# Kernel optimization log

Hardware: AMD Instinct MI355X
Metric: run time of the kernel (lower is better)

## Reference

```python
import jax, jax.numpy as jnp
import numpy as np

B, C, H, W = 32, 256, 32, 32
N_EMBED = 8192
BETA = 0.25  # used for the (unreturned) commitment loss in the original


def setup_inputs() -> dict:
    key = jax.random.key(0)
    k1, k2 = jax.random.split(key)
    z = jax.random.normal(k1, (B, C, H, W), dtype=jnp.float32)
    embedding = jax.random.normal(k2, (N_EMBED, C), dtype=jnp.float32)
    return {"z": z, "embedding": embedding}


def reference(z, embedding):
    # z: [b, c, h, w] -> [b, h, w, c] -> [N, d]
    b, c, h, w = z.shape
    z_bhwc = jnp.transpose(z, (0, 2, 3, 1))
    z_flat = z_bhwc.reshape(-1, c)  # [N, d]

    # Squared L2 distance to every codebook entry: [N, n_embed]
    d = (
        jnp.sum(z_flat * z_flat, axis=1, keepdims=True)
        + jnp.sum(embedding * embedding, axis=1)
        - 2.0 * jnp.einsum("nd,kd->nk", z_flat, embedding)
    )
    min_encoding_indices = jnp.argmin(d, axis=1)  # [N] int

    # Codebook gather + straight-through estimator
    z_q = embedding[min_encoding_indices].reshape(b, h, w, c)
    z_q = z_bhwc + jax.lax.stop_gradient(z_q - z_bhwc)
    z_q = jnp.transpose(z_q, (0, 3, 1, 2))  # back to [b, c, h, w]
    return z_q, min_encoding_indices
```

## Files before the change

kernel.cpp:

```cpp
#include <hip/hip_runtime.h>

#define BATCH   32
#define CDIM    256
#define HWSZ    1024
#define NTOK    32768
#define KEMB    8192
#define ZQ_SIZE (BATCH * CDIM * HWSZ)

typedef short bf16x8 __attribute__((ext_vector_type(8)));
typedef float floatx4 __attribute__((ext_vector_type(4)));

#define MSPLIT 4
#define STRIP  (KEMB / MSPLIT)
#define MB8    128
#define NB8    128
#define MT8    (STRIP / MB8)

#define WS8_ESQ   0ULL
#define WS8_EQM   32768ULL
#define WS8_EH    65536ULL
#define WS8_ZH    4259840ULL
#define WS8_ZL    21037056ULL
#define WS8_PART  37814272ULL
#define WS8_IDX   39911424ULL
#define WS8_TOTAL 40042496ULL

__device__ __forceinline__ unsigned short bf16rne(float f) {
    unsigned int u = __float_as_uint(f);
    return (unsigned short)((u + 0x7fffu + ((u >> 16) & 1u)) >> 16);
}
__device__ __forceinline__ unsigned int packsplit(float f) {
    unsigned int u  = __float_as_uint(f);
    unsigned int hi = (u + 0x7fffu + ((u >> 16) & 1u)) >> 16;
    float rest      = f - __uint_as_float(hi << 16);
    unsigned int u2 = __float_as_uint(rest);
    unsigned int lo = (u2 + 0x7fffu + ((u2 >> 16) & 1u)) >> 16;
    return (hi << 16) | lo;
}
__device__ __forceinline__ unsigned umin32(unsigned a, unsigned b) { return a < b ? a : b; }
__device__ __forceinline__ unsigned umax32(unsigned a, unsigned b) { return a > b ? a : b; }

#define GLOAD_LDS16(g, l) \
    __builtin_amdgcn_global_load_lds((const __attribute__((address_space(1))) void*)(g), \
                                     (__attribute__((address_space(3))) void*)(l), 16, 0, 0)

__global__ void esqcvt_kernel(const float* __restrict__ emb, float* __restrict__ eSq,
                              float* __restrict__ eqm, unsigned short* __restrict__ eh) {
    int k    = blockIdx.x * 4 + (threadIdx.x >> 6);
    int lane = threadIdx.x & 63;
    float4 v = *(const float4*)&emb[k * CDIM + lane * 4];
    float s  = v.x * v.x + v.y * v.y + v.z * v.z + v.w * v.w;
    #pragma unroll
    for (int off = 32; off; off >>= 1) s += __shfl_down(s, off);
    ushort4 h = make_ushort4(bf16rne(v.x), bf16rne(v.y), bf16rne(v.z), bf16rne(v.w));
    *(ushort4*)&eh[k * CDIM + lane * 4] = h;
    if (lane == 0) { eSq[k] = s; eqm[k] = s * 2048.0f + 8388608.0f; }
}

__global__ void splitz_kernel(const float* __restrict__ z, unsigned short* __restrict__ zh,
                              unsigned short* __restrict__ zl) {
    __shared__ unsigned int tile[64][65];
    int b  = blockIdx.x >> 6;
    int r  = blockIdx.x & 63;
    int dt = r >> 4, ht = r & 15;
    int t  = threadIdx.x;
    #pragma unroll
    for (int i = 0; i < 4; ++i) {
        int u  = t + 256 * i;
        int dr = u >> 4;
        int c4 = (u & 15) * 4;
        float4 v = *(const float4*)&z[(((size_t)(b * 256 + dt * 64 + dr)) << 10) + ht * 64 + c4];
        tile[dr][c4 + 0] = packsplit(v.x);
        tile[dr][c4 + 1] = packsplit(v.y);
        tile[dr][c4 + 2] = packsplit(v.z);
        tile[dr][c4 + 3] = packsplit(v.w);
    }
    __syncthreads();
    #pragma unroll
    for (int i = 0; i < 2; ++i) {
        int u  = t + 256 * i;
        int tr = u & 63;
        int d8 = u >> 6;
        unsigned short h8[8], l8[8];
        #pragma unroll
        for (int j = 0; j < 8; ++j) {
            unsigned int p = tile[d8 * 8 + j][tr];
            h8[j] = (unsigned short)(p >> 16);
            l8[j] = (unsigned short)(p & 0xffff);
        }
        size_t off = (size_t)(b * 1024 + ht * 64 + tr) * 256 + dt * 64 + d8 * 8;
        *(uint4*)&zh[off] = *(uint4*)h8;
        *(uint4*)&zl[off] = *(uint4*)l8;
    }
}

#define EQOFF 49152u

#define ISSUE_A(rn, bo_) do { \
    const char* ga_ = gA0 + (size_t)((rn) >> 2) * 65536 + (size_t)((rn) & 3) * 128; \
    _Pragma("unroll") \
    for (int j_ = 0; j_ < 4; ++j_) \
        GLOAD_LDS16(ga_ + j_ * 4096, lds + (bo_) + wvOff + j_ * 1024); \
} while (0)

#define MFMA_ROUND(dr_, bo_) do { \
    __builtin_amdgcn_s_setprio(1); \
    _Pragma("unroll") \
    for (int dk_ = 0; dk_ < 2; ++dk_) { \
        const unsigned xoff_ = (bo_) + (((unsigned)(dk_ * 4) + (unsigned)quad) ^ cx) * 16; \
        bf16x8 afr_[4]; \
        _Pragma("unroll") \
        for (int rf_ = 0; rf_ < 4; ++rf_) afr_[rf_] = *(const bf16x8*)(lds + aR[rf_] + xoff_); \
        _Pragma("unroll") \
        for (int rf_ = 0; rf_ < 4; ++rf_) \
            _Pragma("unroll") \
            for (int cf_ = 0; cf_ < 4; ++cf_) \
                acc[rf_][cf_] = __builtin_amdgcn_mfma_f32_16x16x32_bf16(afr_[rf_], bfr[cf_][dr_][dk_], acc[rf_][cf_], 0, 0, 0); \
    } \
    __builtin_amdgcn_s_setprio(0); \
} while (0)

#define TOP3_EPI(mt_) do { \
    _Pragma("unroll") \
    for (int rf_ = 0; rf_ < 4; ++rf_) { \
        const unsigned base_ = (unsigned)((mt_) * MB8 + wm * 64 + rf_ * 16 + quad * 4); \
        floatx4 eq = *(const floatx4*)(lds + EQOFF + (base_ << 2)); \
        _Pragma("unroll") \
        for (int cf_ = 0; cf_ < 4; ++cf_) { \
            _Pragma("unroll") \
            for (int rr_ = 0; rr_ < 4; ++rr_) { \
                float kf = fmaf(acc[rf_][cf_][rr_], -4096.f, eq[rr_]); \
                unsigned key = (__float_as_uint(kf) << 11) | (base_ + (unsigned)rr_); \
                unsigned m1 = umax32(k1[cf_], key); \
                k1[cf_] = umin32(k1[cf_], key); \
                unsigned m2 = umax32(k2[cf_], m1); \
                k2[cf_] = umin32(k2[cf_], m1); \
                k3[cf_] = umin32(k3[cf_], m2); \
            } \
        } \
    } \
} while (0)

#define VMW4()  asm volatile("s_waitcnt vmcnt(4)" ::: "memory")
#define VMW0()  asm volatile("s_waitcnt vmcnt(0)" ::: "memory")
#define BARR()  asm volatile("s_barrier" ::: "memory")

__global__ __launch_bounds__(256, 2)
void dist8_kernel(const unsigned short* __restrict__ zhp,
                  const unsigned short* __restrict__ ehp,
                  const float* __restrict__ eqm,
                  uint4* __restrict__ part) {
    __shared__ __align__(16) char lds[57344];

    const int t    = threadIdx.x;
    const int lane = t & 63;
    const int wv   = t >> 6;
    const int wm   = wv >> 1, wn = wv & 1;
    const int l15  = lane & 15, quad = lane >> 4;

    const int nb = blockIdx.x & 255;
    const int q  = blockIdx.x >> 8;
    const int n0 = nb * NB8;
    const int cstrip = q * STRIP;

    const int dmaRow  = lane >> 3;
    const int dmaChnk = (lane & 7) ^ dmaRow;
    const unsigned laneGoff = (unsigned)dmaRow * 512 + (unsigned)dmaChnk * 16;

    const char* gA0 = (const char*)ehp + (size_t)(cstrip + wv * 32) * 512 + laneGoff;
    const char* gB0 = (const char*)zhp + (size_t)(n0 + wv * 32) * 512 + laneGoff;
    const unsigned wvOff = (unsigned)wv * 4096;
    const unsigned cx = (unsigned)(l15 & 7);

    bf16x8 bfr[4][4][2];

    #pragma unroll
    for (int s = 0; s < 2; ++s)
        #pragma unroll
        for (int j = 0; j < 4; ++j)
            GLOAD_LDS16(gB0 + s * 128 + j * 4096, lds + s * 16384 + wvOff + j * 1024);
    #pragma unroll
    for (int j = 0; j < 2; ++j)
        GLOAD_LDS16((const char*)(eqm + cstrip) + wv * 2048 + j * 1024 + lane * 16,
                    lds + EQOFF + (unsigned)wv * 2048 + (unsigned)j * 1024);
    __syncthreads();
    #pragma unroll
    for (int cf = 0; cf < 4; ++cf) {
        const unsigned bRow = (unsigned)(wn * 64 + cf * 16 + l15) * 128;
        #pragma unroll
        for (int s = 0; s < 2; ++s)
            #pragma unroll
            for (int dk = 0; dk < 2; ++dk)
                bfr[cf][s][dk] = *(const bf16x8*)(lds + s * 16384 + bRow +
                                    (((unsigned)(dk * 4) + (unsigned)quad) ^ cx) * 16);
    }
    __syncthreads();
    #pragma unroll
    for (int s = 0; s < 2; ++s)
        #pragma unroll
        for (int j = 0; j < 4; ++j)
            GLOAD_LDS16(gB0 + (s + 2) * 128 + j * 4096, lds + s * 16384 + wvOff + j * 1024);
    __syncthreads();
    #pragma unroll
    for (int cf = 0; cf < 4; ++cf) {
        const unsigned bRow = (unsigned)(wn * 64 + cf * 16 + l15) * 128;
        #pragma unroll
        for (int s = 0; s < 2; ++s)
            #pragma unroll
            for (int dk = 0; dk < 2; ++dk)
                bfr[cf][s + 2][dk] = *(const bf16x8*)(lds + s * 16384 + bRow +
                                    (((unsigned)(dk * 4) + (unsigned)quad) ^ cx) * 16);
    }
    __syncthreads();

    unsigned aR[4];
    #pragma unroll
    for (int rf = 0; rf < 4; ++rf) aR[rf] = (unsigned)(wm * 64 + rf * 16 + l15) * 128;

    unsigned k1[4], k2[4], k3[4];
    #pragma unroll
    for (int cf = 0; cf < 4; ++cf) { k1[cf] = 0xFFFFFFFFu; k2[cf] = 0xFFFFFFFFu; k3[cf] = 0xFFFFFFFFu; }

    ISSUE_A(0, 0u);
    ISSUE_A(1, 16384u);

    unsigned bufR = 0u;
    for (int mt = 0; mt < MT8 - 1; ++mt) {
        floatx4 acc[4][4];
        #pragma unroll
        for (int rf = 0; rf < 4; ++rf)
            #pragma unroll
            for (int cf = 0; cf < 4; ++cf) acc[rf][cf] = (floatx4){0.f, 0.f, 0.f, 0.f};

        #pragma unroll
        for (int dr = 0; dr < 4; ++dr) {
            VMW4();
            BARR();
            const unsigned bufI = (bufR == 0u) ? 32768u : bufR - 16384u;
            ISSUE_A(mt * 4 + dr + 2, bufI);
            MFMA_ROUND(dr, bufR);
            bufR = (bufR == 32768u) ? 0u : bufR + 16384u;
        }
        TOP3_EPI(mt);
    }
    {
        floatx4 acc[4][4];
        #pragma unroll
        for (int rf = 0; rf < 4; ++rf)
            #pragma unroll
            for (int cf = 0; cf < 4; ++cf) acc[rf][cf] = (floatx4){0.f, 0.f, 0.f, 0.f};

        VMW4(); BARR();
        { const unsigned bufI = (bufR == 0u) ? 32768u : bufR - 16384u; ISSUE_A(62, bufI); }
        MFMA_ROUND(0, bufR);
        bufR = (bufR == 32768u) ? 0u : bufR + 16384u;

        VMW4(); BARR();
        { const unsigned bufI = (bufR == 0u) ? 32768u : bufR - 16384u; ISSUE_A(63, bufI); }
        MFMA_ROUND(1, bufR);
        bufR = (bufR == 32768u) ? 0u : bufR + 16384u;

        VMW4(); BARR();
        MFMA_ROUND(2, bufR);
        bufR = (bufR == 32768u) ? 0u : bufR + 16384u;

        VMW0(); BARR();
        MFMA_ROUND(3, bufR);

        TOP3_EPI(15);
    }

    #pragma unroll
    for (int cf = 0; cf < 4; ++cf) {
        #pragma unroll
        for (int s = 0; s < 2; ++s) {
            int m = s ? 32 : 16;
            unsigned o1 = (unsigned)__shfl((int)k1[cf], lane ^ m, 64);
            unsigned o2 = (unsigned)__shfl((int)k2[cf], lane ^ m, 64);
            unsigned o3 = (unsigned)__shfl((int)k3[cf], lane ^ m, 64);
            unsigned a1  = umax32(k1[cf], o1);
            k1[cf]       = umin32(k1[cf], o1);
            unsigned b1  = umin32(k2[cf], o2);
            unsigned r3a = umax32(a1, b1);
            k2[cf]       = umin32(a1, b1);
            k3[cf]       = umin32(r3a, umin32(k3[cf], o3));
        }
    }

    __syncthreads();
    uint4* red = (uint4*)lds;
    if (quad == 0) {
        #pragma unroll
        for (int cf = 0; cf < 4; ++cf)
            red[wm * 128 + wn * 64 + cf * 16 + l15] = make_uint4(k1[cf], k2[cf], k3[cf], 0u);
    }
    __syncthreads();
    if (t < 128) {
        uint4 a = red[t], b = red[128 + t];
        unsigned a1  = umax32(a.x, b.x);
        unsigned r1  = umin32(a.x, b.x);
        unsigned b1  = umin32(a.y, b.y);
        unsigned r3a = umax32(a1, b1);
        unsigned r2  = umin32(a1, b1);
        unsigned r3  = umin32(r3a, umin32(a.z, b.z));
        part[q * NTOK + n0 + t] = make_uint4(r1, r2, r3, 0u);
    }
}

__global__ void rescore12_kernel(const unsigned short* __restrict__ zh,
                                 const unsigned short* __restrict__ zl,
                                 const float* __restrict__ emb,
                                 const float* __restrict__ eSq, const uint4* __restrict__ part,
                                 int* __restrict__ idx, float* __restrict__ idxF) {
    int n    = blockIdx.x * 4 + (threadIdx.x >> 6);
    int lane = threadIdx.x & 63;
    int c[12];
    #pragma unroll
    for (int s = 0; s < 4; ++s) {
        uint4 p = part[s * NTOK + n];
        c[3 * s]     = s * STRIP + (int)(p.x & 0x7FFu);
        c[3 * s + 1] = s * STRIP + (int)(p.y & 0x7FFu);
        c[3 * s + 2] = s * STRIP + (int)(p.z & 0x7FFu);
    }
    ushort4 h = *(const ushort4*)&zh[(size_t)n * CDIM + lane * 4];
    ushort4 l = *(const ushort4*)&zl[(size_t)n * CDIM + lane * 4];
    float z0 = __uint_as_float((unsigned)h.x << 16) + __uint_as_float((unsigned)l.x << 16);
    float z1 = __uint_as_float((unsigned)h.y << 16) + __uint_as_float((unsigned)l.y << 16);
    float z2 = __uint_as_float((unsigned)h.z << 16) + __uint_as_float((unsigned)l.z << 16);
    float z3 = __uint_as_float((unsigned)h.w << 16) + __uint_as_float((unsigned)l.w << 16);
    float acc[12];
    #pragma unroll
    for (int s = 0; s < 12; ++s) {
        float4 e = *(const float4*)&emb[(size_t)c[s] * CDIM + lane * 4];
        acc[s] = fmaf(z0, e.x, fmaf(z1, e.y, fmaf(z2, e.z, z3 * e.w)));
    }
    #pragma unroll
    for (int off = 32; off; off >>= 1) {
        #pragma unroll
        for (int s = 0; s < 12; ++s) acc[s] += __shfl_down(acc[s], off);
    }
    if (lane == 0) {
        float bd = 3.4e38f; int bi = 0x7fffffff;
        #pragma unroll
        for (int s = 0; s < 12; ++s) {
            float dv = eSq[c[s]] - 2.f * acc[s];
            if (dv < bd || (dv == bd && c[s] < bi)) { bd = dv; bi = c[s]; }
        }
        idx[n]  = bi;
        idxF[n] = (float)bi;
    }
}

__global__ void gather2_kernel(const float* __restrict__ emb, const int* __restrict__ idx,
                               float* __restrict__ out) {
    __shared__ float tile[32 * 260];
    __shared__ int rows[32];
    const int t  = threadIdx.x;
    const int n0 = blockIdx.x * 32;
    if (t < 32) rows[t] = idx[n0 + t];
    __syncthreads();
    {
        int r  = t >> 3;
        int c0 = (t & 7) * 32;
        const float* src = emb + (size_t)rows[r] * CDIM + c0;
        #pragma unroll
        for (int j = 0; j < 8; ++j) {
            float4 v = *(const float4*)(src + j * 4);
            *(float4*)&tile[r * 260 + c0 + j * 4] = v;
        }
    }
    __syncthreads();
    const int b   = n0 >> 10;
    const int hw0 = n0 & 1023;
    const int cg  = t >> 3;
    const int h4  = (t & 7) * 4;
    #pragma unroll
    for (int j = 0; j < 8; ++j) {
        int c = cg + j * 32;
        float4 v;
        v.x = tile[(h4 + 0) * 260 + c];
        v.y = tile[(h4 + 1) * 260 + c];
        v.z = tile[(h4 + 2) * 260 + c];
        v.w = tile[(h4 + 3) * 260 + c];
        *(float4*)&out[((size_t)b << 18) | ((size_t)c << 10) | (size_t)(hw0 + h4)] = v;
    }
}

#define F_BM  128
#define F_BK  128
#define F_BD  32
#define F_BSS (F_BK + 4)
#define F_KSPLIT 4
#define F_KPER  (KEMB / F_KSPLIT)
#define FWS_ESQ 0
#define FWS_PV  32768
#define FWS_PI  557056
#define FWS_IDX 1081344

__global__ void esq_kernel(const float* __restrict__ emb, float* __restrict__ eSq) {
    int k    = blockIdx.x * 4 + (threadIdx.x >> 6);
    int lane = threadIdx.x & 63;
    float4 v = *(const float4*)&emb[k * CDIM + lane * 4];
    float s  = v.x * v.x + v.y * v.y + v.z * v.z + v.w * v.w;
    #pragma unroll
    for (int off = 32; off; off >>= 1) s += __shfl_down(s, off);
    if (lane == 0) eSq[k] = s;
}

__global__ void dist_kernel(const float* __restrict__ z, const float* __restrict__ emb,
                            const float* __restrict__ eSq,
                            float* __restrict__ pv, int* __restrict__ pi) {
    __shared__ __align__(16) char smem[(F_BD * F_BM + F_BD * F_BSS) * 4];
    float (*As)[F_BM]  = (float (*)[F_BM])smem;
    float (*Bs)[F_BSS] = (float (*)[F_BSS])(smem + F_BD * F_BM * 4);
    const int t = threadIdx.x, tx = t & 15, ty = t >> 4;
    const int rb = blockIdx.x & 255, q = blockIdx.x >> 8;
    const int m0 = rb * F_BM, bb = m0 >> 10, hw0 = m0 & 1023;
    float minv[8]; int mini[8];
    #pragma unroll
    for (int i = 0; i < 8; ++i) { minv[i] = 3.4028235e38f; mini[i] = 0; }
    const int kbeg = q * F_KPER;
    for (int k0 = kbeg; k0 < kbeg + F_KPER; k0 += F_BK) {
        float acc[8][8];
        #pragma unroll
        for (int r = 0; r < 8; ++r)
            #pragma unroll
            for (int c = 0; c < 8; ++c) acc[r][c] = 0.f;
        for (int d0 = 0; d0 < CDIM; d0 += F_BD) {
            __syncthreads();
            #pragma unroll
            for (int i = 0; i < 4; ++i) {
                int u = t + i * 256; int m4 = (u & 31) << 2; int cR = u >> 5;
                float4 v = *(const float4*)&z[(bb << 18) + ((d0 + cR) << 10) + hw0 + m4];
                *(float4*)&As[cR][m4] = v;
            }
            #pragma unroll
            for (int i = 0; i < 4; ++i) {
                int u = t + i * 256; int kR = u >> 3; int c4 = (u & 7) << 2;
                float4 v = *(const float4*)&emb[(k0 + kR) * CDIM + d0 + c4];
                Bs[c4 + 0][kR] = v.x; Bs[c4 + 1][kR] = v.y;
                Bs[c4 + 2][kR] = v.z; Bs[c4 + 3][kR] = v.w;
            }
            __syncthreads();
            #pragma unroll
            for (int d = 0; d < F_BD; ++d) {
                float a[8], bb2[8];
                *(float4*)&a[0] = *(const float4*)&As[d][(ty << 2)];
                *(float4*)&a[4] = *(const float4*)&As[d][64 + (ty << 2)];
                *(float4*)&bb2[0] = *(const float4*)&Bs[d][(tx << 2)];
                *(float4*)&bb2[4] = *(const float4*)&Bs[d][64 + (tx << 2)];
                #pragma unroll
                for (int r = 0; r < 8; ++r)
                    #pragma unroll
                    for (int c = 0; c < 8; ++c) acc[r][c] = fmaf(a[r], bb2[c], acc[r][c]);
            }
        }
        #pragma unroll
        for (int c = 0; c < 8; ++c) {
            int kk = (c < 4) ? ((tx << 2) + c) : (64 + (tx << 2) + (c - 4));
            int kg = k0 + kk;
            float es = eSq[kg];
            #pragma unroll
            for (int r = 0; r < 8; ++r) {
                float v = fmaf(-2.f, acc[r][c], es);
                if (v < minv[r]) { minv[r] = v; mini[r] = kg; }
            }
        }
    }
    __syncthreads();
    float (*redV)[16] = (float (*)[16])smem;
    int   (*redI)[16] = (int   (*)[16])(smem + F_BM * 16 * 4);
    #pragma unroll
    for (int r = 0; r < 8; ++r) {
        int row = (r < 4) ? ((ty << 2) + r) : (64 + (ty << 2) + (r - 4));
        redV[row][tx] = minv[r]; redI[row][tx] = mini[r];
    }
    __syncthreads();
    if (t < F_BM) {
        float bv = redV[t][0]; int bi = redI[t][0];
        #pragma unroll
        for (int i = 1; i < 16; ++i) {
            float v = redV[t][i]; int ii = redI[t][i];
            if (v < bv || (v == bv && ii < bi)) { bv = v; bi = ii; }
        }
        int n = m0 + t;
        pv[q * NTOK + n] = bv; pi[q * NTOK + n] = bi;
    }
}

__global__ void merge_kernel(const float* __restrict__ pv, const int* __restrict__ pi,
                             int* __restrict__ idxOut, float* __restrict__ idxFOut) {
    int n = blockIdx.x * 256 + threadIdx.x;
    float bv = pv[n]; int bi = pi[n];
    #pragma unroll
    for (int q = 1; q < F_KSPLIT; ++q) {
        float v = pv[q * NTOK + n]; int ii = pi[q * NTOK + n];
        if (v < bv || (v == bv && ii < bi)) { bv = v; bi = ii; }
    }
    idxOut[n] = bi; idxFOut[n] = (float)bi;
}

extern "C" void kernel_launch(void* const* d_in, const int* in_sizes, int n_in,
                              void* d_out, int out_size, void* d_ws, size_t ws_size,
                              hipStream_t stream) {
    const float* z   = (const float*)d_in[0];
    const float* emb = (const float*)d_in[1];
    float* out = (float*)d_out;
    char*  ws  = (char*)d_ws;

    if (ws_size >= WS8_TOTAL) {
        float*          eSq  = (float*)(ws + WS8_ESQ);
        float*          eqm  = (float*)(ws + WS8_EQM);
        unsigned short* eh   = (unsigned short*)(ws + WS8_EH);
        unsigned short* zh   = (unsigned short*)(ws + WS8_ZH);
        unsigned short* zl   = (unsigned short*)(ws + WS8_ZL);
        uint4*          part = (uint4*)(ws + WS8_PART);
        int*            idx  = (int*)(ws + WS8_IDX);

        esqcvt_kernel <<<KEMB / 4, 256, 0, stream>>>(emb, eSq, eqm, eh);
        splitz_kernel <<<2048, 256, 0, stream>>>(z, zh, zl);
        dist8_kernel  <<<256 * MSPLIT, 256, 0, stream>>>(zh, eh, eqm, part);
        rescore12_kernel<<<NTOK / 4, 256, 0, stream>>>(zh, zl, emb, eSq, part, idx, out + ZQ_SIZE);
        gather2_kernel<<<NTOK / 32, 256, 0, stream>>>(emb, idx, out);
    } else {
        float* eSq = (float*)(ws + FWS_ESQ);
        float* pv  = (float*)(ws + FWS_PV);
        int*   pi  = (int*)(ws + FWS_PI);
        int*   idx = (int*)(ws + FWS_IDX);
        esq_kernel  <<<KEMB / 4, 256, 0, stream>>>(emb, eSq);
        dist_kernel <<<256 * F_KSPLIT, 256, 0, stream>>>(z, emb, eSq, pv, pi);
        merge_kernel<<<NTOK / 256, 256, 0, stream>>>(pv, pi, idx, out + ZQ_SIZE);
        gather2_kernel<<<NTOK / 32, 256, 0, stream>>>(emb, idx, out);
    }
}
```

Before: 273.9 us.

## Deepen A-tile LDS ring to four buffers and prefetch fragments across barrier

```diff
diff --git a/kernel.cpp b/kernel.cpp
--- a/kernel.cpp
+++ b/kernel.cpp
@@ -94,7 +94,7 @@
     }
 }
 
-#define EQOFF 49152u
+#define EQOFF 65536u
 
 #define ISSUE_A(rn, bo_) do { \
     const char* ga_ = gA0 + (size_t)((rn) >> 2) * 65536 + (size_t)((rn) & 3) * 128; \
@@ -103,21 +103,35 @@
         GLOAD_LDS16(ga_ + j_ * 4096, lds + (bo_) + wvOff + j_ * 1024); \
 } while (0)
 
-#define MFMA_ROUND(dr_, bo_) do { \
+#define PHASE(mt_, dr_, doIssue_, vmN_) do { \
+    const unsigned bufC_ = (unsigned)((dr_) & 3) << 14; \
+    const unsigned bufN_ = (unsigned)(((dr_) + 1) & 3) << 14; \
+    bf16x8 afrB_[4]; \
+    _Pragma("unroll") \
+    for (int rf_ = 0; rf_ < 4; ++rf_) \
+        afrB_[rf_] = *(const bf16x8*)(lds + bufC_ + aR[rf_] + xoff1); \
+    if ((vmN_) == 4) { asm volatile("s_waitcnt vmcnt(4)" ::: "memory"); } \
+    else             { asm volatile("s_waitcnt vmcnt(0)" ::: "memory"); } \
+    __builtin_amdgcn_s_barrier(); \
+    if (doIssue_) ISSUE_A((mt_) * 4 + (dr_) + 3, (unsigned)(((dr_) + 3) & 3) << 14); \
+    bf16x8 afrX_[4]; \
+    _Pragma("unroll") \
+    for (int rf_ = 0; rf_ < 4; ++rf_) \
+        afrX_[rf_] = *(const bf16x8*)(lds + bufN_ + aR[rf_] + xoff0); \
     __builtin_amdgcn_s_setprio(1); \
     _Pragma("unroll") \
-    for (int dk_ = 0; dk_ < 2; ++dk_) { \
-        const unsigned xoff_ = (bo_) + (((unsigned)(dk_ * 4) + (unsigned)quad) ^ cx) * 16; \
-        bf16x8 afr_[4]; \
+    for (int rf_ = 0; rf_ < 4; ++rf_) \
         _Pragma("unroll") \
-        for (int rf_ = 0; rf_ < 4; ++rf_) afr_[rf_] = *(const bf16x8*)(lds + aR[rf_] + xoff_); \
+        for (int cf_ = 0; cf_ < 4; ++cf_) \
+            acc[rf_][cf_] = __builtin_amdgcn_mfma_f32_16x16x32_bf16(afrA[rf_], bfr[cf_][dr_][0], acc[rf_][cf_], 0, 0, 0); \
+    _Pragma("unroll") \
+    for (int rf_ = 0; rf_ < 4; ++rf_) \
         _Pragma("unroll") \
-        for (int rf_ = 0; rf_ < 4; ++rf_) \
-            _Pragma("unroll") \
-            for (int cf_ = 0; cf_ < 4; ++cf_) \
-                acc[rf_][cf_] = __builtin_amdgcn_mfma_f32_16x16x32_bf16(afr_[rf_], bfr[cf_][dr_][dk_], acc[rf_][cf_], 0, 0, 0); \
-    } \
+        for (int cf_ = 0; cf_ < 4; ++cf_) \
+            acc[rf_][cf_] = __builtin_amdgcn_mfma_f32_16x16x32_bf16(afrB_[rf_], bfr[cf_][dr_][1], acc[rf_][cf_], 0, 0, 0); \
     __builtin_amdgcn_s_setprio(0); \
+    _Pragma("unroll") \
+    for (int rf_ = 0; rf_ < 4; ++rf_) afrA[rf_] = afrX_[rf_]; \
 } while (0)
 
 #define TOP3_EPI(mt_) do { \
@@ -141,16 +155,12 @@
     } \
 } while (0)
 
-#define VMW4()  asm volatile("s_waitcnt vmcnt(4)" ::: "memory")
-#define VMW0()  asm volatile("s_waitcnt vmcnt(0)" ::: "memory")
-#define BARR()  asm volatile("s_barrier" ::: "memory")
-
 __global__ __launch_bounds__(256, 2)
 void dist8_kernel(const unsigned short* __restrict__ zhp,
                   const unsigned short* __restrict__ ehp,
                   const float* __restrict__ eqm,
                   uint4* __restrict__ part) {
-    __shared__ __align__(16) char lds[57344];
+    __shared__ __align__(16) char lds[73728];
 
     const int t    = threadIdx.x;
     const int lane = t & 63;
@@ -171,6 +181,8 @@
     const char* gB0 = (const char*)zhp + (size_t)(n0 + wv * 32) * 512 + laneGoff;
     const unsigned wvOff = (unsigned)wv * 4096;
     const unsigned cx = (unsigned)(l15 & 7);
+    const unsigned xoff0 = (((unsigned)quad) ^ cx) * 16;
+    const unsigned xoff1 = ((4u + (unsigned)quad) ^ cx) * 16;
 
     bf16x8 bfr[4][4][2];
 
@@ -188,11 +200,10 @@
     for (int cf = 0; cf < 4; ++cf) {
         const unsigned bRow = (unsigned)(wn * 64 + cf * 16 + l15) * 128;
         #pragma unroll
-        for (int s = 0; s < 2; ++s)
-            #pragma unroll
-            for (int dk = 0; dk < 2; ++dk)
-                bfr[cf][s][dk] = *(const bf16x8*)(lds + s * 16384 + bRow +
-                                    (((unsigned)(dk * 4) + (unsigned)quad) ^ cx) * 16);
+        for (int s = 0; s < 2; ++s) {
+            bfr[cf][s][0] = *(const bf16x8*)(lds + s * 16384 + bRow + xoff0);
+            bfr[cf][s][1] = *(const bf16x8*)(lds + s * 16384 + bRow + xoff1);
+        }
     }
     __syncthreads();
     #pragma unroll
@@ -205,11 +216,10 @@
     for (int cf = 0; cf < 4; ++cf) {
         const unsigned bRow = (unsigned)(wn * 64 + cf * 16 + l15) * 128;
         #pragma unroll
-        for (int s = 0; s < 2; ++s)
-            #pragma unroll
-            for (int dk = 0; dk < 2; ++dk)
-                bfr[cf][s + 2][dk] = *(const bf16x8*)(lds + s * 16384 + bRow +
-                                    (((unsigned)(dk * 4) + (unsigned)quad) ^ cx) * 16);
+        for (int s = 0; s < 2; ++s) {
+            bfr[cf][s + 2][0] = *(const bf16x8*)(lds + s * 16384 + bRow + xoff0);
+            bfr[cf][s + 2][1] = *(const bf16x8*)(lds + s * 16384 + bRow + xoff1);
+        }
     }
     __syncthreads();
 
@@ -223,50 +233,51 @@
 
     ISSUE_A(0, 0u);
     ISSUE_A(1, 16384u);
-
-    unsigned bufR = 0u;
+    ISSUE_A(2, 32768u);
+    asm volatile("s_waitcnt vmcnt(8)" ::: "memory");
+    __builtin_amdgcn_s_barrier();
+    bf16x8 afrA[4];
+    #pragma unroll
+    for (int rf = 0; rf < 4; ++rf) afrA[rf] = *(const bf16x8*)(lds + aR[rf] + xoff0);
+
+    floatx4 acc[4][4];
     for (int mt = 0; mt < MT8 - 1; ++mt) {
-        floatx4 acc[4][4];
         #pragma unroll
         for (int rf = 0; rf < 4; ++rf)
             #pragma unroll
             for (int cf = 0; cf < 4; ++cf) acc[rf][cf] = (floatx4){0.f, 0.f, 0.f, 0.f};
-
-        #pragma unroll
-        for (int dr = 0; dr < 4; ++dr) {
-            VMW4();
-            BARR();
-            const unsigned bufI = (bufR == 0u) ? 32768u : bufR - 16384u;
-            ISSUE_A(mt * 4 + dr + 2, bufI);
-            MFMA_ROUND(dr, bufR);
-            bufR = (bufR == 32768u) ? 0u : bufR + 16384u;
-        }
+        #pragma unroll
+        for (int dr = 0; dr < 4; ++dr)
+            PHASE(mt, dr, 1, 4);
         TOP3_EPI(mt);
     }
     {
-        floatx4 acc[4][4];
         #pragma unroll
         for (int rf = 0; rf < 4; ++rf)
             #pragma unroll
             for (int cf = 0; cf < 4; ++cf) acc[rf][cf] = (floatx4){0.f, 0.f, 0.f, 0.f};
 
-        VMW4(); BARR();
-        { const unsigned bufI = (bufR == 0u) ? 32768u : bufR - 16384u; ISSUE_A(62, bufI); }
-        MFMA_ROUND(0, bufR);
-        bufR = (bufR == 32768u) ? 0u : bufR + 16384u;
-
-        VMW4(); BARR();
-        { const unsigned bufI = (bufR == 0u) ? 32768u : bufR - 16384u; ISSUE_A(63, bufI); }
-        MFMA_ROUND(1, bufR);
-        bufR = (bufR == 32768u) ? 0u : bufR + 16384u;
-
-        VMW4(); BARR();
-        MFMA_ROUND(2, bufR);
-        bufR = (bufR == 32768u) ? 0u : bufR + 16384u;
-
-        VMW0(); BARR();
-        MFMA_ROUND(3, bufR);
-
+        PHASE(15, 0, 1, 4);
+        PHASE(15, 1, 0, 4);
+        PHASE(15, 2, 0, 0);
+        {
+            bf16x8 afrB_[4];
+            #pragma unroll
+            for (int rf = 0; rf < 4; ++rf)
+                afrB_[rf] = *(const bf16x8*)(lds + (3u << 14) + aR[rf] + xoff1);
+            __builtin_amdgcn_s_setprio(1);
+            #pragma unroll
+            for (int rf = 0; rf < 4; ++rf)
+                #pragma unroll
+                for (int cf = 0; cf < 4; ++cf)
+                    acc[rf][cf] = __builtin_amdgcn_mfma_f32_16x16x32_bf16(afrA[rf], bfr[cf][3][0], acc[rf][cf], 0, 0, 0);
+            #pragma unroll
+            for (int rf = 0; rf < 4; ++rf)
+                #pragma unroll
+                for (int cf = 0; cf < 4; ++cf)
+                    acc[rf][cf] = __builtin_amdgcn_mfma_f32_16x16x32_bf16(afrB_[rf], bfr[cf][3][1], acc[rf][cf], 0, 0, 0);
+            __builtin_amdgcn_s_setprio(0);
+        }
         TOP3_EPI(15);
     }
 
```

New measurement: 292.5 us. +6.8%, slower.
